# Kernel tuning notes

Hardware: AMD Instinct MI355X
Metric: run time of the kernel (lower is better)

## Reference

```python
import jax, jax.numpy as jnp
import numpy as np

N = 100000      # nodes
E = 1600000     # directed edges (avg degree 16)
F_IN = 256      # dataset.num_node_features
HID = 64        # hidden
C = 40          # dataset.num_classes


def setup_inputs() -> dict:
    key = jax.random.key(0)
    k0, k1, k2, k3 = jax.random.split(key, 4)
    x = jax.random.normal(k0, (N, F_IN), dtype=jnp.float32)
    edge_index = jax.random.randint(k1, (2, E), 0, N, dtype=jnp.int32)
    # Glorot-style init like GCNConv.reset_parameters
    W1 = jax.random.normal(k2, (F_IN, HID), dtype=jnp.float32) * (1.0 / np.sqrt(F_IN))
    b1 = jnp.zeros((HID,), dtype=jnp.float32)
    W2 = jax.random.normal(k3, (HID, C), dtype=jnp.float32) * (1.0 / np.sqrt(HID))
    b2 = jnp.zeros((C,), dtype=jnp.float32)
    return {"x": x, "edge_index": edge_index, "W1": W1, "b1": b1, "W2": W2, "b2": b2}


def gcn_conv(x, row, col, norm, W, b):
    # PyG GCNConv: out[col] += norm * (x @ W)[row]; then + bias
    n = x.shape[0]
    h = x @ W                                   # [N, out]
    msg = h[row] * norm[:, None]                # [E+N, out] gather + scale
    out = jax.ops.segment_sum(msg, col, num_segments=n)  # scatter-add
    return out + b


def _norm_coeffs(edge_index, n, dtype):
    # add self-loops, then symmetric normalization D^{-1/2} A D^{-1/2}
    loop = jnp.arange(n, dtype=edge_index.dtype)
    row = jnp.concatenate([edge_index[0], loop])
    col = jnp.concatenate([edge_index[1], loop])
    deg = jax.ops.segment_sum(jnp.ones_like(col, dtype=dtype), col, num_segments=n)
    dis = jnp.where(deg > 0, jax.lax.rsqrt(jnp.maximum(deg, 1.0)), 0.0)
    return row, col, dis[row] * dis[col]


def reference(x, edge_index, W1, b1, W2, b2):
    n = x.shape[0]
    row, col, norm = _norm_coeffs(edge_index, n, x.dtype)
    h = jax.nn.relu(gcn_conv(x, row, col, norm, W1, b1))
    # F.dropout(p=0.5, training=False) is identity in eval mode
    out = gcn_conv(h, row, col, norm, W2, b2)
    return jax.nn.log_softmax(out, axis=1)
```

## Files before the change

kernel.cpp:

```cpp
#include <hip/hip_runtime.h>
#include <math.h>

#define N_NODES 100000
#define N_EDGES 1600000
#define F_INDIM 256
#define HID 64
#define NCLS 40
#define NB_SCAN 391
#define NBKT 196
#define BKT_CAP 10240
#define EPB 8192

typedef __attribute__((ext_vector_type(8))) short short8;
typedef __attribute__((ext_vector_type(4))) float floatx4;

__device__ __forceinline__ unsigned short f2bf(float f) {
  unsigned u = __float_as_uint(f);
  unsigned r = (u + 0x7FFFu + ((u >> 16) & 1u)) >> 16;
  return (unsigned short)r;
}
__device__ __forceinline__ float bf2f(unsigned short h) {
  return __uint_as_float(((unsigned)h) << 16);
}
__device__ __forceinline__ void add8(float* a, uint4 u) {
  a[0] += __uint_as_float(u.x << 16);
  a[1] += __uint_as_float(u.x & 0xFFFF0000u);
  a[2] += __uint_as_float(u.y << 16);
  a[3] += __uint_as_float(u.y & 0xFFFF0000u);
  a[4] += __uint_as_float(u.z << 16);
  a[5] += __uint_as_float(u.z & 0xFFFF0000u);
  a[6] += __uint_as_float(u.w << 16);
  a[7] += __uint_as_float(u.w & 0xFFFF0000u);
}


__global__ __launch_bounds__(256) void k_zero(int* __restrict__ gcur,
                                              int* __restrict__ start) {
  int t = threadIdx.x;
  if (t < NBKT) gcur[t] = 0;
  if (t == 0) start[N_NODES] = N_EDGES;
}


__global__ __launch_bounds__(256) void k_binA(const int* __restrict__ row,
                                              const int* __restrict__ col,
                                              int* __restrict__ gcur,
                                              unsigned int* __restrict__ bktdata) {
  __shared__ int hist[NBKT];
  __shared__ int cur[NBKT];
  __shared__ int gbase[NBKT];
  const int t = threadIdx.x;
  const int e0 = blockIdx.x * EPB;
  const int n = min(EPB, N_EDGES - e0);
  if (t < NBKT) hist[t] = 0;
  __syncthreads();
  for (int i = t; i < n; i += 256) atomicAdd(&hist[col[e0 + i] >> 9], 1);
  __syncthreads();
  if (t < NBKT) {
    cur[t] = 0;
    int h = hist[t];
    gbase[t] = (h > 0) ? atomicAdd(&gcur[t], h) : 0;
  }
  __syncthreads();
  for (int i = t; i < n; i += 256) {
    int c = col[e0 + i];
    int r = row[e0 + i];
    int b = c >> 9;
    int p = atomicAdd(&cur[b], 1);
    bktdata[(size_t)b * BKT_CAP + gbase[b] + p] =
        ((unsigned)(c & 511) << 17) | (unsigned)r;
  }
}


__global__ __launch_bounds__(256) void k_histdis(const int* __restrict__ gcur,
                                                 const unsigned int* __restrict__ bktdata,
                                                 int* __restrict__ degi,
                                                 float* __restrict__ dis) {
  __shared__ int h[512];
  const int b = blockIdx.x, t = threadIdx.x;
  h[t] = 0; h[t + 256] = 0;
  __syncthreads();
  const int cnt = gcur[b];
  const unsigned int* p = bktdata + (size_t)b * BKT_CAP;
  for (int i = t; i < cnt; i += 256) atomicAdd(&h[p[i] >> 17], 1);
  __syncthreads();
  int n0 = b * 512 + t;
  if (n0 < N_NODES) { degi[n0] = h[t]; dis[n0] = rsqrtf((float)(h[t] + 1)); }
  int n1 = n0 + 256;
  if (n1 < N_NODES) { degi[n1] = h[t + 256]; dis[n1] = rsqrtf((float)(h[t + 256] + 1)); }
}


__global__ __launch_bounds__(256) void k_scan1(const int* __restrict__ degi,
                                               int* __restrict__ start,
                                               int* __restrict__ bsum) {
  __shared__ int s[256];
  const int t = threadIdx.x;
  const int i = blockIdx.x * 256 + t;
  int v = (i < N_NODES) ? degi[i] : 0;
  s[t] = v;
  __syncthreads();
#pragma unroll
  for (int off = 1; off < 256; off <<= 1) {
    int u = (t >= off) ? s[t - off] : 0;
    __syncthreads();
    s[t] += u;
    __syncthreads();
  }
  if (i < N_NODES) start[i] = s[t] - v;
  if (t == 255) bsum[blockIdx.x] = s[255];
}

__global__ __launch_bounds__(512) void k_scan2(const int* __restrict__ bsum,
                                               int* __restrict__ bsumS) {
  __shared__ int s[512];
  const int t = threadIdx.x;
  int v = (t < NB_SCAN) ? bsum[t] : 0;
  s[t] = v;
  __syncthreads();
#pragma unroll
  for (int off = 1; off < 512; off <<= 1) {
    int u = (t >= off) ? s[t - off] : 0;
    __syncthreads();
    s[t] += u;
    __syncthreads();
  }
  if (t < NB_SCAN) bsumS[t] = s[t] - v;
}

__global__ __launch_bounds__(256) void k_scan3(int* __restrict__ start,
                                               const int* __restrict__ bsumS) {
  int i = blockIdx.x * 256 + threadIdx.x;
  if (i < N_NODES) start[i] += bsumS[blockIdx.x];
}


__global__ __launch_bounds__(256) void k_place(const int* __restrict__ gcur,
                                               const unsigned int* __restrict__ bktdata,
                                               const int* __restrict__ start,
                                               int* __restrict__ esrc) {
  __shared__ int cur[512];
  const int b = blockIdx.x, t = threadIdx.x;
  cur[t] = 0; cur[t + 256] = 0;
  __syncthreads();
  const int cnt = gcur[b];
  const unsigned int* p = bktdata + (size_t)b * BKT_CAP;
  const int nbase = b * 512;
  for (int i = t; i < cnt; i += 256) {
    unsigned u = p[i];
    int ld = u >> 17;
    int src = u & 0x1FFFF;
    int pos = start[nbase + ld] + atomicAdd(&cur[ld], 1);
    esrc[pos] = src;
  }
}


#define KP 264

__global__ __launch_bounds__(256) void k_gemm1(const float* __restrict__ x,
                                               const float* __restrict__ W1,
                                               const float* __restrict__ dis,
                                               unsigned short* __restrict__ h1b) {
  __shared__ unsigned short wt[HID * KP];
  const int tid = threadIdx.x;
  const int lane = tid & 63;
  const int w = tid >> 6;
  const int quad = lane >> 4;
  const int l15 = lane & 15;
  const int rowBase = blockIdx.x * 64;

#pragma unroll
  for (int i = 0; i < 16; ++i) {
    int f = tid + 256 * i;
    int k = f >> 4;
    int n0 = (f & 15) * 4;
    float4 v = *(const float4*)&W1[(size_t)k * HID + n0];
    wt[(n0 + 0) * KP + k] = f2bf(v.x);
    wt[(n0 + 1) * KP + k] = f2bf(v.y);
    wt[(n0 + 2) * KP + k] = f2bf(v.z);
    wt[(n0 + 3) * KP + k] = f2bf(v.w);
  }
  __syncthreads();

  const int ar = rowBase + w * 16 + l15;
  const float* xrow = x + (size_t)((ar < N_NODES) ? ar : N_NODES - 1) * F_INDIM + quad * 8;

  floatx4 acc[4];
#pragma unroll
  for (int c = 0; c < 4; ++c) acc[c] = (floatx4){0.f, 0.f, 0.f, 0.f};

#pragma unroll
  for (int kc = 0; kc < F_INDIM; kc += 32) {
    const float4 va = *(const float4*)(xrow + kc);
    const float4 vb = *(const float4*)(xrow + kc + 4);
    short8 a;
    a[0] = (short)f2bf(va.x); a[1] = (short)f2bf(va.y);
    a[2] = (short)f2bf(va.z); a[3] = (short)f2bf(va.w);
    a[4] = (short)f2bf(vb.x); a[5] = (short)f2bf(vb.y);
    a[6] = (short)f2bf(vb.z); a[7] = (short)f2bf(vb.w);
#pragma unroll
    for (int c = 0; c < 4; ++c) {
      const short8 b = *(const short8*)&wt[(c * 16 + l15) * KP + kc + quad * 8];
      acc[c] = __builtin_amdgcn_mfma_f32_16x16x32_bf16(a, b, acc[c], 0, 0, 0);
    }
  }

#pragma unroll
  for (int reg = 0; reg < 4; ++reg) {
    int gr = rowBase + w * 16 + quad * 4 + reg;
    if (gr < N_NODES) {
      float d = dis[gr];
#pragma unroll
      for (int c = 0; c < 4; ++c)
        h1b[(size_t)gr * HID + c * 16 + l15] = f2bf(d * acc[c][reg]);
    }
  }
}


__global__ __launch_bounds__(256) void k_agg1(const int* __restrict__ esrc,
                                              const int* __restrict__ start,
                                              const float* __restrict__ dis,
                                              const unsigned short* __restrict__ h1b,
                                              const float* __restrict__ b1,
                                              unsigned short* __restrict__ ab) {
  int gid = blockIdx.x * 256 + threadIdx.x;
  int wid = gid >> 6;
  int lane = gid & 63;
  if (wid >= N_NODES) return;
  const int g = lane >> 3;
  const int q = lane & 7;
  const uint4* hp4 = (const uint4*)h1b;
  int i = start[wid];
  const int e1 = start[wid + 1];
  float acc[8];
#pragma unroll
  for (int j = 0; j < 8; ++j) acc[j] = 0.f;
  for (; i + 16 <= e1; i += 16) {
    int sA = esrc[i + g];
    int sB = esrc[i + 8 + g];
    uint4 uA = hp4[(size_t)sA * 8 + q];
    uint4 uB = hp4[(size_t)sB * 8 + q];
    add8(acc, uA);
    add8(acc, uB);
  }
  if (i + 8 <= e1) {
    int s = esrc[i + g];
    uint4 u = hp4[(size_t)s * 8 + q];
    add8(acc, u);
    i += 8;
  }
  int rem = e1 - i;
  if (g < rem) {
    int s = esrc[i + g];
    uint4 u = hp4[(size_t)s * 8 + q];
    add8(acc, u);
  }
#pragma unroll
  for (int off = 8; off < 64; off <<= 1) {
#pragma unroll
    for (int j = 0; j < 8; ++j) acc[j] += __shfl_xor(acc[j], off);
  }
  if (g == 0) {
    uint4 us = hp4[(size_t)wid * 8 + q];
    add8(acc, us);
    float d = dis[wid];
    float4 ba = *(const float4*)&b1[q * 8];
    float4 bb = *(const float4*)&b1[q * 8 + 4];
    float v0 = fmaxf(d * acc[0] + ba.x, 0.f);
    float v1 = fmaxf(d * acc[1] + ba.y, 0.f);
    float v2 = fmaxf(d * acc[2] + ba.z, 0.f);
    float v3 = fmaxf(d * acc[3] + ba.w, 0.f);
    float v4 = fmaxf(d * acc[4] + bb.x, 0.f);
    float v5 = fmaxf(d * acc[5] + bb.y, 0.f);
    float v6 = fmaxf(d * acc[6] + bb.z, 0.f);
    float v7 = fmaxf(d * acc[7] + bb.w, 0.f);
    uint4 o;
    o.x = (unsigned)f2bf(v0) | ((unsigned)f2bf(v1) << 16);
    o.y = (unsigned)f2bf(v2) | ((unsigned)f2bf(v3) << 16);
    o.z = (unsigned)f2bf(v4) | ((unsigned)f2bf(v5) << 16);
    o.w = (unsigned)f2bf(v6) | ((unsigned)f2bf(v7) << 16);
    ((uint4*)ab)[(size_t)wid * 8 + q] = o;
  }
}


#define AP 72

__global__ __launch_bounds__(256) void k_gemm2(const unsigned short* __restrict__ ab,
                                               const float* __restrict__ W2,
                                               const float* __restrict__ dis,
                                               unsigned short* __restrict__ gb) {
  __shared__ unsigned short as[64 * AP];
  __shared__ unsigned short w2t[48 * AP];
  const int tid = threadIdx.x;
  const int lane = tid & 63;
  const int w = tid >> 6;
  const int quad = lane >> 4;
  const int l15 = lane & 15;
  const int rowBase = blockIdx.x * 64;

  for (int i = tid; i < 48 * 64; i += 256) {
    int n = i >> 6;
    int k = i & 63;
    w2t[n * AP + k] = (n < NCLS) ? f2bf(W2[(size_t)k * NCLS + n]) : (unsigned short)0;
  }
#pragma unroll
  for (int i = 0; i < 2; ++i) {
    int f = tid + 256 * i;
    int r = f >> 3;
    int q = f & 7;
    int gr = rowBase + r;
    short8 v = (short8){0, 0, 0, 0, 0, 0, 0, 0};
    if (gr < N_NODES) v = *(const short8*)&ab[(size_t)gr * HID + q * 8];
    *(short8*)&as[r * AP + q * 8] = v;
  }
  __syncthreads();

  floatx4 acc[3];
#pragma unroll
  for (int c = 0; c < 3; ++c) acc[c] = (floatx4){0.f, 0.f, 0.f, 0.f};

#pragma unroll
  for (int kh = 0; kh < 2; ++kh) {
    const short8 a = *(const short8*)&as[(w * 16 + l15) * AP + kh * 32 + quad * 8];
#pragma unroll
    for (int c = 0; c < 3; ++c) {
      const short8 b = *(const short8*)&w2t[(c * 16 + l15) * AP + kh * 32 + quad * 8];
      acc[c] = __builtin_amdgcn_mfma_f32_16x16x32_bf16(a, b, acc[c], 0, 0, 0);
    }
  }

#pragma unroll
  for (int reg = 0; reg < 4; ++reg) {
    int gr = rowBase + w * 16 + quad * 4 + reg;
    if (gr < N_NODES) {
      float d = dis[gr];
#pragma unroll
      for (int c = 0; c < 3; ++c) {
        int cc = c * 16 + l15;
        gb[(size_t)gr * 64 + cc] = f2bf(d * acc[c][reg]);
      }
      gb[(size_t)gr * 64 + 48 + l15] = 0;
    }
  }
}


__global__ __launch_bounds__(256) void k_agg2ls(const int* __restrict__ esrc,
                                                const int* __restrict__ start,
                                                const float* __restrict__ dis,
                                                const unsigned short* __restrict__ gb,
                                                const float* __restrict__ b2,
                                                float* __restrict__ out) {
  int gid = blockIdx.x * 256 + threadIdx.x;
  int node = gid >> 6;
  int lane = gid & 63;
  if (node >= N_NODES) return;
  const int g = lane >> 3;
  const int q = lane & 7;
  const uint4* gp4 = (const uint4*)gb;
  int i = start[node];
  const int e1 = start[node + 1];
  float acc[8];
#pragma unroll
  for (int j = 0; j < 8; ++j) acc[j] = 0.f;
  for (; i + 16 <= e1; i += 16) {
    int sA = esrc[i + g];
    int sB = esrc[i + 8 + g];
    uint4 uA = gp4[(size_t)sA * 8 + q];
    uint4 uB = gp4[(size_t)sB * 8 + q];
    add8(acc, uA);
    add8(acc, uB);
  }
  if (i + 8 <= e1) {
    int s = esrc[i + g];
    uint4 u = gp4[(size_t)s * 8 + q];
    add8(acc, u);
    i += 8;
  }
  int rem = e1 - i;
  if (g < rem) {
    int s = esrc[i + g];
    uint4 u = gp4[(size_t)s * 8 + q];
    add8(acc, u);
  }
#pragma unroll
  for (int off = 8; off < 64; off <<= 1) {
#pragma unroll
    for (int j = 0; j < 8; ++j) acc[j] += __shfl_xor(acc[j], off);
  }
  const bool wr = (g == 0) && (q < 5);
  float v0 = 0.f, v1 = 0.f, v2 = 0.f, v3 = 0.f, v4 = 0.f, v5 = 0.f, v6 = 0.f, v7 = 0.f;
  float m = -INFINITY;
  if (g == 0) {
    uint4 us = gp4[(size_t)node * 8 + q];
    add8(acc, us);
  }
  if (wr) {
    float d = dis[node];
    float4 ba = *(const float4*)&b2[q * 8];
    float4 bb = *(const float4*)&b2[q * 8 + 4];
    v0 = d * acc[0] + ba.x;
    v1 = d * acc[1] + ba.y;
    v2 = d * acc[2] + ba.z;
    v3 = d * acc[3] + ba.w;
    v4 = d * acc[4] + bb.x;
    v5 = d * acc[5] + bb.y;
    v6 = d * acc[6] + bb.z;
    v7 = d * acc[7] + bb.w;
    m = fmaxf(fmaxf(fmaxf(v0, v1), fmaxf(v2, v3)),
              fmaxf(fmaxf(v4, v5), fmaxf(v6, v7)));
  }
#pragma unroll
  for (int off = 1; off < 8; off <<= 1) m = fmaxf(m, __shfl_xor(m, off));
  float el = 0.f;
  if (wr) {
    el = __expf(v0 - m) + __expf(v1 - m) + __expf(v2 - m) + __expf(v3 - m) +
         __expf(v4 - m) + __expf(v5 - m) + __expf(v6 - m) + __expf(v7 - m);
  }
#pragma unroll
  for (int off = 1; off < 8; off <<= 1) el += __shfl_xor(el, off);
  float ls = logf(el);
  if (wr) {
    float4 o1 = make_float4(v0 - m - ls, v1 - m - ls, v2 - m - ls, v3 - m - ls);
    float4 o2 = make_float4(v4 - m - ls, v5 - m - ls, v6 - m - ls, v7 - m - ls);
    *(float4*)&out[(size_t)node * NCLS + q * 8] = o1;
    *(float4*)&out[(size_t)node * NCLS + q * 8 + 4] = o2;
  }
}


extern "C" void kernel_launch(void* const* d_in, const int* in_sizes, int n_in,
                              void* d_out, int out_size, void* d_ws, size_t ws_size,
                              hipStream_t stream) {
  const float* x  = (const float*)d_in[0];
  const int*   ei = (const int*)d_in[1];
  const float* W1 = (const float*)d_in[2];
  const float* b1 = (const float*)d_in[3];
  const float* W2 = (const float*)d_in[4];
  const float* b2 = (const float*)d_in[5];
  float* out = (float*)d_out;

  const int* row = ei;
  const int* col = ei + N_EDGES;

  int*            esrc    = (int*)d_ws;
  unsigned int*   bktdata = (unsigned int*)(esrc + N_EDGES);
  unsigned short* h1b     = (unsigned short*)(bktdata + (size_t)NBKT * BKT_CAP);
  unsigned short* ab      = h1b + (size_t)N_NODES * HID;
  float*          dis     = (float*)(ab + (size_t)N_NODES * HID);
  int*            degi    = (int*)(dis + N_NODES);
  int*            start   = degi + N_NODES;
  int*            gcur    = start + N_NODES + 1;
  int*            bsum    = gcur + NBKT;
  int*            bsumS   = bsum + NB_SCAN;
  unsigned short* gb      = h1b;

  k_zero<<<1, 256, 0, stream>>>(gcur, start);
  k_binA<<<(N_EDGES + EPB - 1) / EPB, 256, 0, stream>>>(row, col, gcur, bktdata);
  k_histdis<<<NBKT, 256, 0, stream>>>(gcur, bktdata, degi, dis);
  k_scan1<<<NB_SCAN, 256, 0, stream>>>(degi, start, bsum);
  k_scan2<<<1, 512, 0, stream>>>(bsum, bsumS);
  k_scan3<<<NB_SCAN, 256, 0, stream>>>(start, bsumS);
  k_place<<<NBKT, 256, 0, stream>>>(gcur, bktdata, start, esrc);

  k_gemm1<<<(N_NODES + 63) / 64, 256, 0, stream>>>(x, W1, dis, h1b);
  k_agg1<<<(N_NODES * 64 + 255) / 256, 256, 0, stream>>>(esrc, start, dis, h1b, b1, ab);

  k_gemm2<<<(N_NODES + 63) / 64, 256, 0, stream>>>(ab, W2, dis, gb);
  k_agg2ls<<<(N_NODES * 64 + 255) / 256, 256, 0, stream>>>(esrc, start, dis, gb, b2, out);
}
```

Baseline: 356.8 us.

## Fuse degree scan into bucket kernels and map eight lanes per node in aggregation

The per-bucket histogram kernel now does a 512-wide local exclusive scan in shared memory. A single small kernel scans the 196 bucket totals, and the placement kernel combines the two to write the start offsets. This replaces the three-kernel global scan and drops the degree array. Both aggregation kernels switch from one 64-lane wave per node to 8 lanes per node, each walking its edges serially two at a time. That removes the cross-group shuffle reduction and the idle lanes on short rows, at the cost of fewer loads in flight per node.

```diff
diff --git a/kernel.cpp b/kernel.cpp
--- a/kernel.cpp
+++ b/kernel.cpp
@@ -6,7 +6,6 @@
 #define F_INDIM 256
 #define HID 64
 #define NCLS 40
-#define NB_SCAN 391
 #define NBKT 196
 #define BKT_CAP 10240
 #define EPB 8192
@@ -75,7 +74,7 @@
 
 __global__ __launch_bounds__(256) void k_histdis(const int* __restrict__ gcur,
                                                  const unsigned int* __restrict__ bktdata,
-                                                 int* __restrict__ degi,
+                                                 int* __restrict__ lscan,
                                                  float* __restrict__ dis) {
   __shared__ int h[512];
   const int b = blockIdx.x, t = threadIdx.x;
@@ -85,20 +84,28 @@
   const unsigned int* p = bktdata + (size_t)b * BKT_CAP;
   for (int i = t; i < cnt; i += 256) atomicAdd(&h[p[i] >> 17], 1);
   __syncthreads();
-  int n0 = b * 512 + t;
-  if (n0 < N_NODES) { degi[n0] = h[t]; dis[n0] = rsqrtf((float)(h[t] + 1)); }
-  int n1 = n0 + 256;
-  if (n1 < N_NODES) { degi[n1] = h[t + 256]; dis[n1] = rsqrtf((float)(h[t + 256] + 1)); }
-}
-
-
-__global__ __launch_bounds__(256) void k_scan1(const int* __restrict__ degi,
-                                               int* __restrict__ start,
-                                               int* __restrict__ bsum) {
+  const int n0 = b * 512 + t, n1 = n0 + 256;
+  const int c0 = h[t], c1 = h[t + 256];
+  if (n0 < N_NODES) dis[n0] = rsqrtf((float)(c0 + 1));
+  if (n1 < N_NODES) dis[n1] = rsqrtf((float)(c1 + 1));
+#pragma unroll
+  for (int off = 1; off < 512; off <<= 1) {
+    int u0 = (t >= off) ? h[t - off] : 0;
+    int u1 = ((t + 256) >= off) ? h[t + 256 - off] : 0;
+    __syncthreads();
+    h[t] += u0; h[t + 256] += u1;
+    __syncthreads();
+  }
+  if (n0 < N_NODES) lscan[n0] = h[t] - c0;
+  if (n1 < N_NODES) lscan[n1] = h[t + 256] - c1;
+}
+
+
+__global__ __launch_bounds__(256) void k_scan2(const int* __restrict__ gcur,
+                                               int* __restrict__ bsumS) {
   __shared__ int s[256];
   const int t = threadIdx.x;
-  const int i = blockIdx.x * 256 + t;
-  int v = (i < N_NODES) ? degi[i] : 0;
+  int v = (t < NBKT) ? gcur[t] : 0;
   s[t] = v;
   __syncthreads();
 #pragma unroll
@@ -108,50 +115,35 @@
     s[t] += u;
     __syncthreads();
   }
-  if (i < N_NODES) start[i] = s[t] - v;
-  if (t == 255) bsum[blockIdx.x] = s[255];
-}
-
-__global__ __launch_bounds__(512) void k_scan2(const int* __restrict__ bsum,
-                                               int* __restrict__ bsumS) {
-  __shared__ int s[512];
-  const int t = threadIdx.x;
-  int v = (t < NB_SCAN) ? bsum[t] : 0;
-  s[t] = v;
-  __syncthreads();
-#pragma unroll
-  for (int off = 1; off < 512; off <<= 1) {
-    int u = (t >= off) ? s[t - off] : 0;
-    __syncthreads();
-    s[t] += u;
-    __syncthreads();
-  }
-  if (t < NB_SCAN) bsumS[t] = s[t] - v;
-}
-
-__global__ __launch_bounds__(256) void k_scan3(int* __restrict__ start,
-                                               const int* __restrict__ bsumS) {
-  int i = blockIdx.x * 256 + threadIdx.x;
-  if (i < N_NODES) start[i] += bsumS[blockIdx.x];
+  if (t < NBKT) bsumS[t] = s[t] - v;
 }
 
 
 __global__ __launch_bounds__(256) void k_place(const int* __restrict__ gcur,
                                                const unsigned int* __restrict__ bktdata,
-                                               const int* __restrict__ start,
+                                               const int* __restrict__ lscan,
+                                               const int* __restrict__ bsumS,
+                                               int* __restrict__ start,
                                                int* __restrict__ esrc) {
   __shared__ int cur[512];
+  __shared__ int sbase[512];
   const int b = blockIdx.x, t = threadIdx.x;
+  const int base = bsumS[b];
+  const int n0 = b * 512 + t, n1 = n0 + 256;
+  int s0 = ((n0 < N_NODES) ? lscan[n0] : 0) + base;
+  int s1 = ((n1 < N_NODES) ? lscan[n1] : 0) + base;
+  sbase[t] = s0; sbase[t + 256] = s1;
+  if (n0 < N_NODES) start[n0] = s0;
+  if (n1 < N_NODES) start[n1] = s1;
   cur[t] = 0; cur[t + 256] = 0;
   __syncthreads();
   const int cnt = gcur[b];
   const unsigned int* p = bktdata + (size_t)b * BKT_CAP;
-  const int nbase = b * 512;
   for (int i = t; i < cnt; i += 256) {
     unsigned u = p[i];
     int ld = u >> 17;
     int src = u & 0x1FFFF;
-    int pos = start[nbase + ld] + atomicAdd(&cur[ld], 1);
+    int pos = sbase[ld] + atomicAdd(&cur[ld], 1);
     esrc[pos] = src;
   }
 }
@@ -227,63 +219,46 @@
                                               const float* __restrict__ b1,
                                               unsigned short* __restrict__ ab) {
   int gid = blockIdx.x * 256 + threadIdx.x;
-  int wid = gid >> 6;
-  int lane = gid & 63;
-  if (wid >= N_NODES) return;
-  const int g = lane >> 3;
-  const int q = lane & 7;
+  int node = gid >> 3;
+  int q = gid & 7;
+  if (node >= N_NODES) return;
   const uint4* hp4 = (const uint4*)h1b;
-  int i = start[wid];
-  const int e1 = start[wid + 1];
+  int i = start[node];
+  const int e1 = start[node + 1];
   float acc[8];
 #pragma unroll
   for (int j = 0; j < 8; ++j) acc[j] = 0.f;
-  for (; i + 16 <= e1; i += 16) {
-    int sA = esrc[i + g];
-    int sB = esrc[i + 8 + g];
-    uint4 uA = hp4[(size_t)sA * 8 + q];
-    uint4 uB = hp4[(size_t)sB * 8 + q];
-    add8(acc, uA);
-    add8(acc, uB);
-  }
-  if (i + 8 <= e1) {
-    int s = esrc[i + g];
-    uint4 u = hp4[(size_t)s * 8 + q];
+  for (; i + 2 <= e1; i += 2) {
+    int s0 = esrc[i];
+    int s1 = esrc[i + 1];
+    uint4 u0 = hp4[(size_t)s0 * 8 + q];
+    uint4 u1 = hp4[(size_t)s1 * 8 + q];
+    add8(acc, u0);
+    add8(acc, u1);
+  }
+  if (i < e1) {
+    uint4 u = hp4[(size_t)esrc[i] * 8 + q];
     add8(acc, u);
-    i += 8;
-  }
-  int rem = e1 - i;
-  if (g < rem) {
-    int s = esrc[i + g];
-    uint4 u = hp4[(size_t)s * 8 + q];
-    add8(acc, u);
-  }
-#pragma unroll
-  for (int off = 8; off < 64; off <<= 1) {
-#pragma unroll
-    for (int j = 0; j < 8; ++j) acc[j] += __shfl_xor(acc[j], off);
-  }
-  if (g == 0) {
-    uint4 us = hp4[(size_t)wid * 8 + q];
-    add8(acc, us);
-    float d = dis[wid];
-    float4 ba = *(const float4*)&b1[q * 8];
-    float4 bb = *(const float4*)&b1[q * 8 + 4];
-    float v0 = fmaxf(d * acc[0] + ba.x, 0.f);
-    float v1 = fmaxf(d * acc[1] + ba.y, 0.f);
-    float v2 = fmaxf(d * acc[2] + ba.z, 0.f);
-    float v3 = fmaxf(d * acc[3] + ba.w, 0.f);
-    float v4 = fmaxf(d * acc[4] + bb.x, 0.f);
-    float v5 = fmaxf(d * acc[5] + bb.y, 0.f);
-    float v6 = fmaxf(d * acc[6] + bb.z, 0.f);
-    float v7 = fmaxf(d * acc[7] + bb.w, 0.f);
-    uint4 o;
-    o.x = (unsigned)f2bf(v0) | ((unsigned)f2bf(v1) << 16);
-    o.y = (unsigned)f2bf(v2) | ((unsigned)f2bf(v3) << 16);
-    o.z = (unsigned)f2bf(v4) | ((unsigned)f2bf(v5) << 16);
-    o.w = (unsigned)f2bf(v6) | ((unsigned)f2bf(v7) << 16);
-    ((uint4*)ab)[(size_t)wid * 8 + q] = o;
-  }
+  }
+  uint4 us = hp4[(size_t)node * 8 + q];
+  add8(acc, us);
+  float d = dis[node];
+  float4 ba = *(const float4*)&b1[q * 8];
+  float4 bb = *(const float4*)&b1[q * 8 + 4];
+  float v0 = fmaxf(d * acc[0] + ba.x, 0.f);
+  float v1 = fmaxf(d * acc[1] + ba.y, 0.f);
+  float v2 = fmaxf(d * acc[2] + ba.z, 0.f);
+  float v3 = fmaxf(d * acc[3] + ba.w, 0.f);
+  float v4 = fmaxf(d * acc[4] + bb.x, 0.f);
+  float v5 = fmaxf(d * acc[5] + bb.y, 0.f);
+  float v6 = fmaxf(d * acc[6] + bb.z, 0.f);
+  float v7 = fmaxf(d * acc[7] + bb.w, 0.f);
+  uint4 o;
+  o.x = (unsigned)f2bf(v0) | ((unsigned)f2bf(v1) << 16);
+  o.y = (unsigned)f2bf(v2) | ((unsigned)f2bf(v3) << 16);
+  o.z = (unsigned)f2bf(v4) | ((unsigned)f2bf(v5) << 16);
+  o.w = (unsigned)f2bf(v6) | ((unsigned)f2bf(v7) << 16);
+  ((uint4*)ab)[(size_t)node * 8 + q] = o;
 }
 
 
@@ -356,49 +331,32 @@
                                                 const float* __restrict__ b2,
                                                 float* __restrict__ out) {
   int gid = blockIdx.x * 256 + threadIdx.x;
-  int node = gid >> 6;
-  int lane = gid & 63;
+  int node = gid >> 3;
+  int q = gid & 7;
   if (node >= N_NODES) return;
-  const int g = lane >> 3;
-  const int q = lane & 7;
   const uint4* gp4 = (const uint4*)gb;
   int i = start[node];
   const int e1 = start[node + 1];
   float acc[8];
 #pragma unroll
   for (int j = 0; j < 8; ++j) acc[j] = 0.f;
-  for (; i + 16 <= e1; i += 16) {
-    int sA = esrc[i + g];
-    int sB = esrc[i + 8 + g];
-    uint4 uA = gp4[(size_t)sA * 8 + q];
-    uint4 uB = gp4[(size_t)sB * 8 + q];
-    add8(acc, uA);
-    add8(acc, uB);
-  }
-  if (i + 8 <= e1) {
-    int s = esrc[i + g];
-    uint4 u = gp4[(size_t)s * 8 + q];
+  for (; i + 2 <= e1; i += 2) {
+    int s0 = esrc[i];
+    int s1 = esrc[i + 1];
+    uint4 u0 = gp4[(size_t)s0 * 8 + q];
+    uint4 u1 = gp4[(size_t)s1 * 8 + q];
+    add8(acc, u0);
+    add8(acc, u1);
+  }
+  if (i < e1) {
+    uint4 u = gp4[(size_t)esrc[i] * 8 + q];
     add8(acc, u);
-    i += 8;
-  }
-  int rem = e1 - i;
-  if (g < rem) {
-    int s = esrc[i + g];
-    uint4 u = gp4[(size_t)s * 8 + q];
-    add8(acc, u);
-  }
-#pragma unroll
-  for (int off = 8; off < 64; off <<= 1) {
-#pragma unroll
-    for (int j = 0; j < 8; ++j) acc[j] += __shfl_xor(acc[j], off);
-  }
-  const bool wr = (g == 0) && (q < 5);
+  }
+  uint4 us = gp4[(size_t)node * 8 + q];
+  add8(acc, us);
+  const bool wr = q < 5;
   float v0 = 0.f, v1 = 0.f, v2 = 0.f, v3 = 0.f, v4 = 0.f, v5 = 0.f, v6 = 0.f, v7 = 0.f;
   float m = -INFINITY;
-  if (g == 0) {
-    uint4 us = gp4[(size_t)node * 8 + q];
-    add8(acc, us);
-  }
   if (wr) {
     float d = dis[node];
     float4 ba = *(const float4*)&b2[q * 8];
@@ -452,24 +410,21 @@
   unsigned short* h1b     = (unsigned short*)(bktdata + (size_t)NBKT * BKT_CAP);
   unsigned short* ab      = h1b + (size_t)N_NODES * HID;
   float*          dis     = (float*)(ab + (size_t)N_NODES * HID);
-  int*            degi    = (int*)(dis + N_NODES);
-  int*            start   = degi + N_NODES;
+  int*            lscan   = (int*)(dis + N_NODES);
+  int*            start   = lscan + N_NODES;
   int*            gcur    = start + N_NODES + 1;
-  int*            bsum    = gcur + NBKT;
-  int*            bsumS   = bsum + NB_SCAN;
+  int*            bsumS   = gcur + NBKT;
   unsigned short* gb      = h1b;
 
   k_zero<<<1, 256, 0, stream>>>(gcur, start);
   k_binA<<<(N_EDGES + EPB - 1) / EPB, 256, 0, stream>>>(row, col, gcur, bktdata);
-  k_histdis<<<NBKT, 256, 0, stream>>>(gcur, bktdata, degi, dis);
-  k_scan1<<<NB_SCAN, 256, 0, stream>>>(degi, start, bsum);
-  k_scan2<<<1, 512, 0, stream>>>(bsum, bsumS);
-  k_scan3<<<NB_SCAN, 256, 0, stream>>>(start, bsumS);
-  k_place<<<NBKT, 256, 0, stream>>>(gcur, bktdata, start, esrc);
+  k_histdis<<<NBKT, 256, 0, stream>>>(gcur, bktdata, lscan, dis);
+  k_scan2<<<1, 256, 0, stream>>>(gcur, bsumS);
+  k_place<<<NBKT, 256, 0, stream>>>(gcur, bktdata, lscan, bsumS, start, esrc);
 
   k_gemm1<<<(N_NODES + 63) / 64, 256, 0, stream>>>(x, W1, dis, h1b);
-  k_agg1<<<(N_NODES * 64 + 255) / 256, 256, 0, stream>>>(esrc, start, dis, h1b, b1, ab);
+  k_agg1<<<(N_NODES * 8 + 255) / 256, 256, 0, stream>>>(esrc, start, dis, h1b, b1, ab);
 
   k_gemm2<<<(N_NODES + 63) / 64, 256, 0, stream>>>(ab, W2, dis, gb);
-  k_agg2ls<<<(N_NODES * 64 + 255) / 256, 256, 0, stream>>>(esrc, start, dis, gb, b2, out);
-}
+  k_agg2ls<<<(N_NODES * 8 + 255) / 256, 256, 0, stream>>>(esrc, start, dis, gb, b2, out);
+}
```

New measurement: 325.2 us. 1.1x faster.
